# Kernel optimization log

Hardware: AMD Instinct MI355X
Metric: run time of the kernel (lower is better)

Reference implementation:

```python
import jax, jax.numpy as jnp
import numpy as np

B, S, D, H = 4, 4096, 128, 128

def setup_inputs() -> dict:
    key = jax.random.key(0)
    ks = jax.random.split(key, 7)
    sd = 1.0 / np.sqrt(D)
    return {
        "x": jax.random.normal(ks[0], (B, S, D), dtype=jnp.float32),
        "Wq": jax.random.normal(ks[1], (D, H), dtype=jnp.float32) * sd,
        "bq": jax.random.normal(ks[2], (H,), dtype=jnp.float32) * sd,
        "Wk": jax.random.normal(ks[3], (D, H), dtype=jnp.float32) * sd,
        "bk": jax.random.normal(ks[4], (H,), dtype=jnp.float32) * sd,
        "Wv": jax.random.normal(ks[5], (D, D), dtype=jnp.float32) * sd,
        "bv": jax.random.normal(ks[6], (D,), dtype=jnp.float32) * sd,
    }

def reference(x, Wq, bq, Wk, bk, Wv, bv):
    # Q,K: [B,S,H]; V: [B,S,D]
    Q = jnp.einsum('bsd,dh->bsh', x, Wq) + bq
    K = jnp.einsum('bsd,dh->bsh', x, Wk) + bk
    V = jnp.einsum('bsd,de->bse', x, Wv) + bv
    scale = jnp.sqrt(jnp.asarray(H, dtype=x.dtype))
    scores = jnp.einsum('bqh,bkh->bqk', Q, K) / scale  # [B,S,S]
    attn = jax.nn.softmax(scores, axis=-1)             # dropout = identity (eval mode)
    context = jnp.einsum('bqk,bkd->bqd', attn, V)      # [B,S,D]
    return context.mean(axis=1)                        # [B,D]
```

## Files before the change

kernel.cpp:

```cpp
#include <hip/hip_runtime.h>

#define SLEN 4096
#define DDIM 128
#define BATCH 4
#define KROWS 256
#define NKB (SLEN / KROWS)
#define QROWS 512
#define NQR (SLEN / QROWS)
#define NW 8
#define SCLOG2E 0.12751743f

typedef __bf16 v8bf __attribute__((ext_vector_type(8)));
typedef float f32x4 __attribute__((ext_vector_type(4)));

__device__ __forceinline__ f32x4 mfma16(v8bf a, v8bf b, f32x4 c) {
  return __builtin_amdgcn_mfma_f32_16x16x32_bf16(a, b, c, 0, 0, 0);
}

__device__ __forceinline__ void gload_lds16(const void* g, void* l) {
  __builtin_amdgcn_global_load_lds(
      (const __attribute__((address_space(1))) unsigned int*)g,
      (__attribute__((address_space(3))) unsigned int*)l, 16, 0, 0);
}

__device__ __forceinline__ void decode_bid(int bid, int& b, int& qr, int& kblk) {
  int x = bid & 7;
  int i = bid >> 3;
  int p = x * 4 + (i >> 4);
  kblk = i & 15;
  b = p >> 3;
  qr = p & 7;
}

__device__ __forceinline__ void stage_kslab(const __bf16* __restrict__ Krow0,
                                            char* buf, int wave, int lane) {
#pragma unroll
  for (int it = 0; it < 8; ++it) {
    int s = it * 512 + wave * 64 + lane;
    int r = s >> 4;
    int pp = s & 15;
    int lsl = pp ^ (r & 7);
    const __bf16* src = Krow0 + (size_t)r * DDIM + lsl * 8;
    char* dst = buf + (size_t)(it * 512 + wave * 64) * 16;
    gload_lds16(src, dst);
  }
}

__global__ __launch_bounds__(256) void k0_wt(const float* __restrict__ Wq,
                                             const float* __restrict__ Wk,
                                             __bf16* __restrict__ Wt) {
  int idx = blockIdx.x * 256 + threadIdx.x;
  int ct = idx >> 8;
  int hs = (idx >> 6) & 3;
  int l  = idx & 63;
  int col = ((ct & 7) << 4) + (l & 15);
  const float* W = (ct < 8) ? Wq : Wk;
  int hbase = hs * 32 + (l >> 4) * 8;
  __bf16* dst = Wt + (size_t)idx * 8;
  for (int i = 0; i < 8; ++i)
    dst[i] = (__bf16)W[(hbase + i) * DDIM + col];
}

__global__ __launch_bounds__(256) void k1_proj(const float* __restrict__ x,
                                               const __bf16* __restrict__ Wt,
                                               const float* __restrict__ bq,
                                               const float* __restrict__ bk,
                                               __bf16* __restrict__ Qb,
                                               __bf16* __restrict__ Kb) {
  int wave = threadIdx.x >> 6, lane = threadIdx.x & 63;
  int lr = lane & 15, lg = lane >> 4;
  int r0 = blockIdx.x * 64 + wave * 16;
  const float* xrow = x + (size_t)(r0 + lr) * DDIM;

  v8bf xf[4];
#pragma unroll
  for (int hs = 0; hs < 4; ++hs) {
    float4 a = *reinterpret_cast<const float4*>(xrow + hs * 32 + lg * 8);
    float4 c = *reinterpret_cast<const float4*>(xrow + hs * 32 + lg * 8 + 4);
    v8bf t;
    t[0] = (__bf16)a.x; t[1] = (__bf16)a.y; t[2] = (__bf16)a.z; t[3] = (__bf16)a.w;
    t[4] = (__bf16)c.x; t[5] = (__bf16)c.y; t[6] = (__bf16)c.z; t[7] = (__bf16)c.w;
    xf[hs] = t;
  }

  for (int ct = 0; ct < 16; ++ct) {
    f32x4 acc = {0.f, 0.f, 0.f, 0.f};
#pragma unroll
    for (int hs = 0; hs < 4; ++hs) {
      v8bf wf = *reinterpret_cast<const v8bf*>(Wt + ((size_t)(ct * 4 + hs) * 64 + lane) * 8);
      acc = mfma16(xf[hs], wf, acc);
    }
    int col = ((ct & 7) << 4) + lr;
    float bias = (ct < 8) ? bq[col] : bk[col];
    __bf16* dst = (ct < 8) ? Qb : Kb;
#pragma unroll
    for (int j = 0; j < 4; ++j) {
      int row = r0 + lg * 4 + j;
      dst[(size_t)row * DDIM + col] = (__bf16)(acc[j] + bias);
    }
  }
}

__global__ __launch_bounds__(512, 4) void k2a_z(const __bf16* __restrict__ Qb,
                                                const __bf16* __restrict__ Kb,
                                                float* __restrict__ zpart) {
  int b, qr, kblk;
  decode_bid(blockIdx.x, b, qr, kblk);
  int p = b * NQR + qr;
  int wave = threadIdx.x >> 6, lane = threadIdx.x & 63;
  int lr = lane & 15, lg = lane >> 4;

  __shared__ __align__(16) char kbuf[KROWS * 256];

  stage_kslab(Kb + ((size_t)b * SLEN + kblk * KROWS) * DDIM, kbuf, wave, lane);
  __syncthreads();

  int qloc0 = wave * 64;
  const __bf16* Qp = Qb + ((size_t)b * SLEN + qr * QROWS + qloc0) * DDIM;

  v8bf qf[4][4];
#pragma unroll
  for (int qs = 0; qs < 4; ++qs)
#pragma unroll
    for (int hs = 0; hs < 4; ++hs)
      qf[qs][hs] = *reinterpret_cast<const v8bf*>(Qp + (size_t)(qs * 16 + lr) * DDIM + hs * 32 + lg * 8);

  float zacc[4][4];
#pragma unroll
  for (int qs = 0; qs < 4; ++qs)
#pragma unroll
    for (int j = 0; j < 4; ++j) zacc[qs][j] = 0.f;

#pragma unroll 2
  for (int kt = 0; kt < KROWS / 16; ++kt) {
    int rowbase = (kt * 16 + lr) * 256;
    f32x4 acc[4];
#pragma unroll
    for (int qs = 0; qs < 4; ++qs) acc[qs] = (f32x4){0.f, 0.f, 0.f, 0.f};
#pragma unroll
    for (int hs = 0; hs < 4; ++hs) {
      int slot = (hs * 4 + lg) ^ (lr & 7);
      v8bf kc = *reinterpret_cast<const v8bf*>(kbuf + rowbase + slot * 16);
#pragma unroll
      for (int qs = 0; qs < 4; ++qs) acc[qs] = mfma16(qf[qs][hs], kc, acc[qs]);
    }
#pragma unroll
    for (int qs = 0; qs < 4; ++qs)
#pragma unroll
      for (int j = 0; j < 4; ++j)
        zacc[qs][j] += exp2f(acc[qs][j] * SCLOG2E);
  }

#pragma unroll
  for (int qs = 0; qs < 4; ++qs)
#pragma unroll
    for (int j = 0; j < 4; ++j) {
      float z = zacc[qs][j];
      z += __shfl_xor(z, 1);
      z += __shfl_xor(z, 2);
      z += __shfl_xor(z, 4);
      z += __shfl_xor(z, 8);
      if (lr == 0)
        zpart[((size_t)p * NKB + kblk) * QROWS + qloc0 + qs * 16 + lg * 4 + j] = z;
    }
}

__global__ __launch_bounds__(512, 4) void k2c_w(const __bf16* __restrict__ Qb,
                                                const __bf16* __restrict__ Kb,
                                                const float* __restrict__ zpart,
                                                float* __restrict__ wpart) {
  int b, qr, kblk;
  decode_bid(blockIdx.x, b, qr, kblk);
  int p = b * NQR + qr;
  int wave = threadIdx.x >> 6, lane = threadIdx.x & 63;
  int lr = lane & 15, lg = lane >> 4;

  __shared__ __align__(16) char kbuf[KROWS * 256];
  __shared__ float invZ[QROWS];
  __shared__ float warr[NW][KROWS];

  stage_kslab(Kb + ((size_t)b * SLEN + kblk * KROWS) * DDIM, kbuf, wave, lane);

  {
    int q = threadIdx.x;
    const float* zp = zpart + (size_t)p * NKB * QROWS + q;
    float z = 0.f;
#pragma unroll
    for (int kb = 0; kb < NKB; ++kb) z += zp[(size_t)kb * QROWS];
    invZ[q] = 1.0f / z;
  }
  __syncthreads();

  int qloc0 = wave * 64;
  const __bf16* Qp = Qb + ((size_t)b * SLEN + qr * QROWS + qloc0) * DDIM;

  v8bf qf[4][4];
#pragma unroll
  for (int qs = 0; qs < 4; ++qs)
#pragma unroll
    for (int hs = 0; hs < 4; ++hs)
      qf[qs][hs] = *reinterpret_cast<const v8bf*>(Qp + (size_t)(qs * 16 + lr) * DDIM + hs * 32 + lg * 8);

  float iz[4][4];
#pragma unroll
  for (int qs = 0; qs < 4; ++qs)
#pragma unroll
    for (int j = 0; j < 4; ++j)
      iz[qs][j] = invZ[qloc0 + qs * 16 + lg * 4 + j];

  float wkacc[KROWS / 16];
#pragma unroll
  for (int kt = 0; kt < KROWS / 16; ++kt) wkacc[kt] = 0.f;

#pragma unroll 2
  for (int kt = 0; kt < KROWS / 16; ++kt) {
    int rowbase = (kt * 16 + lr) * 256;
    f32x4 acc[4];
#pragma unroll
    for (int qs = 0; qs < 4; ++qs) acc[qs] = (f32x4){0.f, 0.f, 0.f, 0.f};
#pragma unroll
    for (int hs = 0; hs < 4; ++hs) {
      int slot = (hs * 4 + lg) ^ (lr & 7);
      v8bf kc = *reinterpret_cast<const v8bf*>(kbuf + rowbase + slot * 16);
#pragma unroll
      for (int qs = 0; qs < 4; ++qs) acc[qs] = mfma16(qf[qs][hs], kc, acc[qs]);
    }
    float wk = 0.f;
#pragma unroll
    for (int qs = 0; qs < 4; ++qs)
#pragma unroll
      for (int j = 0; j < 4; ++j)
        wk += exp2f(acc[qs][j] * SCLOG2E) * iz[qs][j];
    wkacc[kt] += wk;
  }

#pragma unroll
  for (int kt = 0; kt < KROWS / 16; ++kt) {
    float wv = wkacc[kt];
    wv += __shfl_xor(wv, 16);
    wv += __shfl_xor(wv, 32);
    if (lg == 0) warr[wave][kt * 16 + lr] = wv;
  }
  __syncthreads();
  if (threadIdx.x < KROWS) {
    int k = threadIdx.x;
    float s = 0.f;
#pragma unroll
    for (int w = 0; w < NW; ++w) s += warr[w][k];
    wpart[(size_t)p * SLEN + kblk * KROWS + k] = s;
  }
}

__global__ __launch_bounds__(128) void k4_u(const float* __restrict__ x,
                                            const float* __restrict__ wpart,
                                            float* __restrict__ upart) {
  int b = blockIdx.y, c = blockIdx.x, d = threadIdx.x;
  __shared__ float ws[128];
  const float* pw = wpart + (size_t)b * NQR * SLEN + c * 128 + d;
  float s = 0.f;
#pragma unroll
  for (int j = 0; j < NQR; ++j) s += pw[(size_t)j * SLEN];
  ws[d] = s;
  __syncthreads();
  const float* xb = x + ((size_t)b * SLEN + c * 128) * DDIM;
  float acc = 0.f;
  for (int kk = 0; kk < 128; ++kk)
    acc += ws[kk] * xb[(size_t)kk * DDIM + d];
  upart[((size_t)b * 32 + c) * DDIM + d] = acc;
}

__global__ __launch_bounds__(128) void k5_out(const float* __restrict__ upart,
                                              const float* __restrict__ Wv,
                                              const float* __restrict__ bv,
                                              float* __restrict__ out) {
  int b = blockIdx.x, d = threadIdx.x;
  __shared__ float u[DDIM];
  float s = 0.f;
  for (int c = 0; c < 32; ++c) s += upart[((size_t)b * 32 + c) * DDIM + d];
  u[d] = s;
  __syncthreads();
  float acc = 0.f;
  for (int dp = 0; dp < DDIM; ++dp) acc += u[dp] * Wv[(size_t)dp * DDIM + d];
  out[b * DDIM + d] = acc * (1.0f / SLEN) + bv[d];
}

extern "C" void kernel_launch(void* const* d_in, const int* in_sizes, int n_in,
                              void* d_out, int out_size, void* d_ws, size_t ws_size,
                              hipStream_t stream) {
  const float* x  = (const float*)d_in[0];
  const float* Wq = (const float*)d_in[1];
  const float* bq = (const float*)d_in[2];
  const float* Wk = (const float*)d_in[3];
  const float* bk = (const float*)d_in[4];
  const float* Wv = (const float*)d_in[5];
  const float* bv = (const float*)d_in[6];
  float* out = (float*)d_out;

  char* ws = (char*)d_ws;
  __bf16* Qb    = (__bf16*)(ws);
  __bf16* Kb    = (__bf16*)(ws + (4u << 20));
  __bf16* Wt    = (__bf16*)(ws + (8u << 20));
  float*  zpart = (float*)(ws + (8u << 20) + (64u << 10));
  float*  wpart = (float*)(ws + (9u << 20) + (64u << 10));
  float*  upart = (float*)(ws + (10u << 20));

  k0_wt  <<<16, 256, 0, stream>>>(Wq, Wk, Wt);
  k1_proj<<<256, 256, 0, stream>>>(x, Wt, bq, bk, Qb, Kb);
  k2a_z  <<<NKB * NQR * BATCH, 512, 0, stream>>>(Qb, Kb, zpart);
  k2c_w  <<<NKB * NQR * BATCH, 512, 0, stream>>>(Qb, Kb, zpart, wpart);
  k4_u   <<<dim3(32, BATCH), 128, 0, stream>>>(x, wpart, upart);
  k5_out <<<BATCH, 128, 0, stream>>>(upart, Wv, bv, out);
}
```

Measured before the change: 83.03 us.

## Halve query tile, fold softmax scale into Q, software-pipeline MFMA and exp

Shrinks the per-block query tile from 512 to 256 rows, which doubles the number of blocks and gives each wave 32 query rows instead of 64. The tile loops become explicitly double-buffered so the MFMA for the next key tile is issued while the exp2 of the previous one runs. The softmax scale times log2(e) is now applied once when Q is written in the projection kernel, so the per-element multiply disappears from both attention passes. The cost is more blocks, each re-staging the K slab with less reuse per stage, and larger zpart/wpart buffers. The upart offset is moved so it does not overlap the larger wpart buffer.

```diff
diff --git a/kernel.cpp b/kernel.cpp
--- a/kernel.cpp
+++ b/kernel.cpp
@@ -5,7 +5,7 @@
 #define BATCH 4
 #define KROWS 256
 #define NKB (SLEN / KROWS)
-#define QROWS 512
+#define QROWS 256
 #define NQR (SLEN / QROWS)
 #define NW 8
 #define SCLOG2E 0.12751743f
@@ -26,10 +26,10 @@
 __device__ __forceinline__ void decode_bid(int bid, int& b, int& qr, int& kblk) {
   int x = bid & 7;
   int i = bid >> 3;
-  int p = x * 4 + (i >> 4);
+  int pr = x * 8 + (i >> 4);
   kblk = i & 15;
-  b = p >> 3;
-  qr = p & 7;
+  b = pr >> 4;
+  qr = pr & 15;
 }
 
 __device__ __forceinline__ void stage_kslab(const __bf16* __restrict__ Krow0,
@@ -44,6 +44,28 @@
     char* dst = buf + (size_t)(it * 512 + wave * 64) * 16;
     gload_lds16(src, dst);
   }
+}
+
+__device__ __forceinline__ void compute_tile(const char* kbuf, const v8bf qf[2][4],
+                                             int lr, int lg, int kt, f32x4 A[2]) {
+  int rowbase = (kt * 16 + lr) * 256;
+#pragma unroll
+  for (int qs = 0; qs < 2; ++qs) A[qs] = (f32x4){0.f, 0.f, 0.f, 0.f};
+#pragma unroll
+  for (int hs = 0; hs < 4; ++hs) {
+    int slot = (hs * 4 + lg) ^ (lr & 7);
+    v8bf kc = *reinterpret_cast<const v8bf*>(kbuf + rowbase + slot * 16);
+#pragma unroll
+    for (int qs = 0; qs < 2; ++qs) A[qs] = mfma16(qf[qs][hs], kc, A[qs]);
+  }
+}
+
+__device__ __forceinline__ void consume_z(const f32x4 A[2], float zacc[2][4]) {
+#pragma unroll
+  for (int qs = 0; qs < 2; ++qs)
+#pragma unroll
+    for (int j = 0; j < 4; ++j)
+      zacc[qs][j] += exp2f(A[qs][j]);
 }
 
 __global__ __launch_bounds__(256) void k0_wt(const float* __restrict__ Wq,
@@ -92,11 +114,12 @@
     }
     int col = ((ct & 7) << 4) + lr;
     float bias = (ct < 8) ? bq[col] : bk[col];
+    float sc   = (ct < 8) ? SCLOG2E : 1.0f;
     __bf16* dst = (ct < 8) ? Qb : Kb;
 #pragma unroll
     for (int j = 0; j < 4; ++j) {
       int row = r0 + lg * 4 + j;
-      dst[(size_t)row * DDIM + col] = (__bf16)(acc[j] + bias);
+      dst[(size_t)row * DDIM + col] = (__bf16)((acc[j] + bias) * sc);
     }
   }
 }
@@ -113,46 +136,40 @@
   __shared__ __align__(16) char kbuf[KROWS * 256];
 
   stage_kslab(Kb + ((size_t)b * SLEN + kblk * KROWS) * DDIM, kbuf, wave, lane);
-  __syncthreads();
-
-  int qloc0 = wave * 64;
+
+  int qloc0 = wave * 32;
   const __bf16* Qp = Qb + ((size_t)b * SLEN + qr * QROWS + qloc0) * DDIM;
 
-  v8bf qf[4][4];
-#pragma unroll
-  for (int qs = 0; qs < 4; ++qs)
+  v8bf qf[2][4];
+#pragma unroll
+  for (int qs = 0; qs < 2; ++qs)
 #pragma unroll
     for (int hs = 0; hs < 4; ++hs)
       qf[qs][hs] = *reinterpret_cast<const v8bf*>(Qp + (size_t)(qs * 16 + lr) * DDIM + hs * 32 + lg * 8);
 
-  float zacc[4][4];
-#pragma unroll
-  for (int qs = 0; qs < 4; ++qs)
+  float zacc[2][4];
+#pragma unroll
+  for (int qs = 0; qs < 2; ++qs)
 #pragma unroll
     for (int j = 0; j < 4; ++j) zacc[qs][j] = 0.f;
 
-#pragma unroll 2
-  for (int kt = 0; kt < KROWS / 16; ++kt) {
-    int rowbase = (kt * 16 + lr) * 256;
-    f32x4 acc[4];
-#pragma unroll
-    for (int qs = 0; qs < 4; ++qs) acc[qs] = (f32x4){0.f, 0.f, 0.f, 0.f};
-#pragma unroll
-    for (int hs = 0; hs < 4; ++hs) {
-      int slot = (hs * 4 + lg) ^ (lr & 7);
-      v8bf kc = *reinterpret_cast<const v8bf*>(kbuf + rowbase + slot * 16);
-#pragma unroll
-      for (int qs = 0; qs < 4; ++qs) acc[qs] = mfma16(qf[qs][hs], kc, acc[qs]);
-    }
-#pragma unroll
-    for (int qs = 0; qs < 4; ++qs)
-#pragma unroll
-      for (int j = 0; j < 4; ++j)
-        zacc[qs][j] += exp2f(acc[qs][j] * SCLOG2E);
-  }
-
-#pragma unroll
-  for (int qs = 0; qs < 4; ++qs)
+  __syncthreads();
+
+  f32x4 a0[2], a1[2];
+  compute_tile(kbuf, qf, lr, lg, 0, a0);
+#pragma unroll 1
+  for (int i = 0; i < 7; ++i) {
+    compute_tile(kbuf, qf, lr, lg, 2 * i + 1, a1);
+    consume_z(a0, zacc);
+    compute_tile(kbuf, qf, lr, lg, 2 * i + 2, a0);
+    consume_z(a1, zacc);
+  }
+  compute_tile(kbuf, qf, lr, lg, 15, a1);
+  consume_z(a0, zacc);
+  consume_z(a1, zacc);
+
+#pragma unroll
+  for (int qs = 0; qs < 2; ++qs)
 #pragma unroll
     for (int j = 0; j < 4; ++j) {
       float z = zacc[qs][j];
@@ -181,66 +198,57 @@
 
   stage_kslab(Kb + ((size_t)b * SLEN + kblk * KROWS) * DDIM, kbuf, wave, lane);
 
-  {
-    int q = threadIdx.x;
-    const float* zp = zpart + (size_t)p * NKB * QROWS + q;
+  if (threadIdx.x < QROWS) {
+    const float* zp = zpart + (size_t)p * NKB * QROWS + threadIdx.x;
     float z = 0.f;
 #pragma unroll
     for (int kb = 0; kb < NKB; ++kb) z += zp[(size_t)kb * QROWS];
-    invZ[q] = 1.0f / z;
-  }
-  __syncthreads();
-
-  int qloc0 = wave * 64;
+    invZ[threadIdx.x] = 1.0f / z;
+  }
+  __syncthreads();
+
+  int qloc0 = wave * 32;
   const __bf16* Qp = Qb + ((size_t)b * SLEN + qr * QROWS + qloc0) * DDIM;
 
-  v8bf qf[4][4];
-#pragma unroll
-  for (int qs = 0; qs < 4; ++qs)
+  v8bf qf[2][4];
+#pragma unroll
+  for (int qs = 0; qs < 2; ++qs)
 #pragma unroll
     for (int hs = 0; hs < 4; ++hs)
       qf[qs][hs] = *reinterpret_cast<const v8bf*>(Qp + (size_t)(qs * 16 + lr) * DDIM + hs * 32 + lg * 8);
 
-  float iz[4][4];
-#pragma unroll
-  for (int qs = 0; qs < 4; ++qs)
+  float iz[2][4];
+#pragma unroll
+  for (int qs = 0; qs < 2; ++qs)
 #pragma unroll
     for (int j = 0; j < 4; ++j)
       iz[qs][j] = invZ[qloc0 + qs * 16 + lg * 4 + j];
 
-  float wkacc[KROWS / 16];
-#pragma unroll
-  for (int kt = 0; kt < KROWS / 16; ++kt) wkacc[kt] = 0.f;
-
-#pragma unroll 2
-  for (int kt = 0; kt < KROWS / 16; ++kt) {
-    int rowbase = (kt * 16 + lr) * 256;
-    f32x4 acc[4];
-#pragma unroll
-    for (int qs = 0; qs < 4; ++qs) acc[qs] = (f32x4){0.f, 0.f, 0.f, 0.f};
-#pragma unroll
-    for (int hs = 0; hs < 4; ++hs) {
-      int slot = (hs * 4 + lg) ^ (lr & 7);
-      v8bf kc = *reinterpret_cast<const v8bf*>(kbuf + rowbase + slot * 16);
-#pragma unroll
-      for (int qs = 0; qs < 4; ++qs) acc[qs] = mfma16(qf[qs][hs], kc, acc[qs]);
-    }
+  auto consume_w = [&](const f32x4 A[2], int kt) {
     float wk = 0.f;
 #pragma unroll
-    for (int qs = 0; qs < 4; ++qs)
+    for (int qs = 0; qs < 2; ++qs)
 #pragma unroll
       for (int j = 0; j < 4; ++j)
-        wk += exp2f(acc[qs][j] * SCLOG2E) * iz[qs][j];
-    wkacc[kt] += wk;
-  }
-
-#pragma unroll
-  for (int kt = 0; kt < KROWS / 16; ++kt) {
-    float wv = wkacc[kt];
-    wv += __shfl_xor(wv, 16);
-    wv += __shfl_xor(wv, 32);
-    if (lg == 0) warr[wave][kt * 16 + lr] = wv;
-  }
+        wk += exp2f(A[qs][j]) * iz[qs][j];
+    wk += __shfl_xor(wk, 16);
+    wk += __shfl_xor(wk, 32);
+    if (lg == 0) warr[wave][kt * 16 + lr] = wk;
+  };
+
+  f32x4 a0[2], a1[2];
+  compute_tile(kbuf, qf, lr, lg, 0, a0);
+#pragma unroll 1
+  for (int i = 0; i < 7; ++i) {
+    compute_tile(kbuf, qf, lr, lg, 2 * i + 1, a1);
+    consume_w(a0, 2 * i);
+    compute_tile(kbuf, qf, lr, lg, 2 * i + 2, a0);
+    consume_w(a1, 2 * i + 1);
+  }
+  compute_tile(kbuf, qf, lr, lg, 15, a1);
+  consume_w(a0, 14);
+  consume_w(a1, 15);
+
   __syncthreads();
   if (threadIdx.x < KROWS) {
     int k = threadIdx.x;
@@ -302,7 +310,7 @@
   __bf16* Wt    = (__bf16*)(ws + (8u << 20));
   float*  zpart = (float*)(ws + (8u << 20) + (64u << 10));
   float*  wpart = (float*)(ws + (9u << 20) + (64u << 10));
-  float*  upart = (float*)(ws + (10u << 20));
+  float*  upart = (float*)(ws + (10u << 20) + (64u << 10));
 
   k0_wt  <<<16, 256, 0, stream>>>(Wq, Wk, Wt);
   k1_proj<<<256, 256, 0, stream>>>(x, Wt, bq, bk, Qb, Kb);
```

Result: faster. 78.73 us (-5.2%).
